# Kernel tuning notes

Hardware: AMD Instinct MI355X
Metric: run time of the kernel (lower is better)

The kernel has to match this reference:

```python
import jax, jax.numpy as jnp
import numpy as np

N = 200000   # gaussians
M = 10000    # scaffold nodes
K = 16       # skinning knn
T = 40       # time steps
F = 32       # semantic feature dim
MAX_S = 0.1
MIN_S = 0.0
EPS = 1e-8


def _qnorm(q):
    return q / jnp.clip(jnp.linalg.norm(q, axis=-1, keepdims=True), 1e-12)


def q2R(q):
    # quaternion (w, x, y, z) -> rotation matrix, normalizing first (matches q2R in source)
    q = _qnorm(q)
    w, x, y, z = q[..., 0], q[..., 1], q[..., 2], q[..., 3]
    r0 = jnp.stack([1 - 2 * (y * y + z * z), 2 * (x * y - w * z), 2 * (x * z + w * y)], -1)
    r1 = jnp.stack([2 * (x * y + w * z), 1 - 2 * (x * x + z * z), 2 * (y * z - w * x)], -1)
    r2 = jnp.stack([2 * (x * z - w * y), 2 * (y * z + w * x), 1 - 2 * (x * x + y * y)], -1)
    return jnp.stack([r0, r1, r2], -2)


def quat_mul(a, b):
    aw, ax, ay, az = a[..., 0], a[..., 1], a[..., 2], a[..., 3]
    bw, bx, by, bz = b[..., 0], b[..., 1], b[..., 2], b[..., 3]
    return jnp.stack([
        aw * bw - ax * bx - ay * by - az * bz,
        aw * bx + ax * bw + ay * bz - az * by,
        aw * by - ax * bz + ay * bw + az * bx,
        aw * bz + ax * by - ay * bx + az * bw], -1)


def quat_conj(q):
    return q * jnp.array([1.0, -1.0, -1.0, -1.0], q.dtype)


def setup_inputs() -> dict:
    key = jax.random.key(0)
    ks = jax.random.split(key, 13)
    return {
        "gs_xyz": 0.05 * jax.random.normal(ks[0], (N, 3), jnp.float32),
        "gs_rotation": jax.random.normal(ks[1], (N, 4), jnp.float32),
        "gs_scaling": jax.random.normal(ks[2], (N, 3), jnp.float32),
        "gs_opacity": jax.random.normal(ks[3], (N, 1), jnp.float32),
        "feat_dc": jax.random.normal(ks[4], (N, 3), jnp.float32),
        "feat_rest": jax.random.normal(ks[5], (N, 9), jnp.float32),
        "node_xyz": jax.random.normal(ks[6], (T, M, 3), jnp.float32),
        "node_quat": jax.random.normal(ks[7], (T, M, 4), jnp.float32),
        "node_sigma": 0.1 + 0.5 * jax.random.uniform(ks[8], (M, 1), jnp.float32),
        "node_sem": jax.random.normal(ks[9], (M, F), jnp.float32),
        "attach_ind": jax.random.randint(ks[10], (N,), 0, M, jnp.int32),
        "ref_time": jax.random.randint(ks[11], (N,), 0, T, jnp.int32),
        "topo_knn": jax.random.randint(ks[12], (M, K), 0, M, jnp.int32),
        "t": 5,
    }


def reference(gs_xyz, gs_rotation, gs_scaling, gs_opacity, feat_dc, feat_rest,
              node_xyz, node_quat, node_sigma, node_sem,
              attach_ind, ref_time, topo_knn, t):
    # --- per-gaussian activated attributes ---
    s = MIN_S + jax.nn.sigmoid(gs_scaling) * (MAX_S - MIN_S)   # s_act
    o = jax.nn.sigmoid(gs_opacity)                              # o_act
    sph = jnp.concatenate([feat_dc, feat_rest], axis=-1)        # [N, 12], full sph order

    # --- leaf-local -> world at ref time (get_xyz / get_R_mtx) ---
    ref_p_attach = node_xyz[ref_time, attach_ind]               # [N,3] async knn gather
    ref_q_attach = node_quat[ref_time, attach_ind]              # [N,4]
    R_ref_attach = q2R(ref_q_attach)                            # [N,3,3]
    x_world = jnp.einsum('nij,nj->ni', R_ref_attach, gs_xyz) + ref_p_attach
    R_world = jnp.einsum('nij,njk->nik', R_ref_attach, q2R(gs_rotation))

    # --- scf.warp: KNN skinning from per-point ref time to target time t ---
    sk_ind = topo_knn[attach_ind]                               # [N,K] neighbor node ids
    p_ref = node_xyz[ref_time[:, None], sk_ind]                 # [N,K,3]
    q_ref = node_quat[ref_time[:, None], sk_ind]                # [N,K,4]
    p_live = node_xyz[t][sk_ind]                                # [N,K,3]
    q_live = node_quat[t][sk_ind]                               # [N,K,4]
    sigma = node_sigma[sk_ind, 0]                               # [N,K]

    diff = x_world[:, None, :] - p_ref                          # [N,K,3]
    dsq = jnp.sum(diff * diff, axis=-1)                         # [N,K]
    w = jnp.exp(-dsq / (2.0 * sigma * sigma + EPS))             # RBF skinning weights
    w = w / (jnp.sum(w, axis=-1, keepdims=True) + EPS)          # [N,K]

    # per-node relative transform ref -> live
    q_rel = quat_mul(_qnorm(q_live), quat_conj(_qnorm(q_ref)))  # [N,K,4]
    R_rel = q2R(q_rel)                                          # [N,K,3,3]
    mu_k = jnp.einsum('nkij,nkj->nki', R_rel, diff) + p_live    # [N,K,3]
    mu_live = jnp.einsum('nk,nki->ni', w, mu_k)                 # [N,3]

    q_blend = jnp.einsum('nk,nkd->nd', w, q_rel)                # blended quaternion
    fr_live = jnp.einsum('nij,njk->nik', q2R(q_blend), R_world) # [N,3,3]

    sem_live = jnp.einsum('nk,nkf->nf', w, node_sem[sk_ind])    # [N,F]

    return mu_live, fr_live, s, o, sph, sem_live
```

## Files before the change

kernel.cpp:

```cpp
#include <hip/hip_runtime.h>

#define KNN 16
#define FSEM 32
#define LPG 4
#define NXCD 8

__device__ __forceinline__ float sigmoidf_(float x) { return 1.0f / (1.0f + __expf(-x)); }

__device__ __forceinline__ void quat_to_R(float qw, float qx, float qy, float qz, float* R) {
    float d = qw * qw + qx * qx + qy * qy + qz * qz;
    float inv = rsqrtf(fmaxf(d, 1e-24f));
    float w = qw * inv, x = qx * inv, y = qy * inv, z = qz * inv;
    R[0] = 1.f - 2.f * (y * y + z * z); R[1] = 2.f * (x * y - w * z); R[2] = 2.f * (x * z + w * y);
    R[3] = 2.f * (x * y + w * z); R[4] = 1.f - 2.f * (x * x + z * z); R[5] = 2.f * (y * z - w * x);
    R[6] = 2.f * (x * z - w * y); R[7] = 2.f * (y * z + w * x); R[8] = 1.f - 2.f * (x * x + y * y);
}

__global__ void __launch_bounds__(256)
k_pack(const float* __restrict__ node_xyz, const float* __restrict__ node_quat,
       const float* __restrict__ node_sigma,
       float* __restrict__ packed, int* __restrict__ cnt, int TM, int M, int B)
{
    int p = blockIdx.x * blockDim.x + threadIdx.x;
    if (p < B && cnt) cnt[p] = 0;
    if (p >= TM) return;
    const int node = p - (p / M) * M;
    const float* x = node_xyz + 3 * (size_t)p;
    float4 a = make_float4(x[0], x[1], x[2], node_sigma[node]);
    float4 q = reinterpret_cast<const float4*>(node_quat)[p];
    float4* dst = reinterpret_cast<float4*>(packed + 8 * (size_t)p);
    dst[0] = a;
    dst[1] = q;
}

__global__ void __launch_bounds__(256)
k_hist(const int* __restrict__ attach, const int* __restrict__ rtime,
       int* __restrict__ cnt, int* __restrict__ rank, int N, int M)
{
    int n = blockIdx.x * blockDim.x + threadIdx.x;
    if (n >= N) return;
    const int key = rtime[n] * M + attach[n];
    rank[n] = atomicAdd(&cnt[key], 1);
}

__global__ void __launch_bounds__(256)
k_scan1(int* __restrict__ cnt, int* __restrict__ blk, int B)
{
    __shared__ int sh[256];
    const int i = blockIdx.x * 256 + threadIdx.x;
    int v = (i < B) ? cnt[i] : 0;
    sh[threadIdx.x] = v;
    __syncthreads();
    int acc = v;
#pragma unroll
    for (int off = 1; off < 256; off <<= 1) {
        int u = (threadIdx.x >= off) ? sh[threadIdx.x - off] : 0;
        __syncthreads();
        acc += u;
        sh[threadIdx.x] = acc;
        __syncthreads();
    }
    if (i < B) cnt[i] = acc - v;
    if (threadIdx.x == 255) blk[blockIdx.x] = acc;
}

__global__ void __launch_bounds__(256)
k_scan2(int* __restrict__ blk, int nblk)
{
    __shared__ int sh[256];
    __shared__ int carry_s;
    if (threadIdx.x == 0) carry_s = 0;
    __syncthreads();
    for (int base = 0; base < nblk; base += 256) {
        const int i = base + threadIdx.x;
        int v = (i < nblk) ? blk[i] : 0;
        sh[threadIdx.x] = v;
        __syncthreads();
        int acc = v;
#pragma unroll
        for (int off = 1; off < 256; off <<= 1) {
            int u = (threadIdx.x >= off) ? sh[threadIdx.x - off] : 0;
            __syncthreads();
            acc += u;
            sh[threadIdx.x] = acc;
            __syncthreads();
        }
        const int carry = carry_s;
        if (i < nblk) blk[i] = acc - v + carry;
        __syncthreads();
        if (threadIdx.x == 255) carry_s = carry + acc;
        __syncthreads();
    }
}

__global__ void __launch_bounds__(256)
k_scatter(const int* __restrict__ attach, const int* __restrict__ rtime,
          const float* __restrict__ gs_xyz,
          const int* __restrict__ rank, const int* __restrict__ cnt,
          const int* __restrict__ blk, float4* __restrict__ meta, int N, int M)
{
    int n = blockIdx.x * blockDim.x + threadIdx.x;
    if (n >= N) return;
    const int a = attach[n], rt = rtime[n];
    const int key = rt * M + a;
    const int pos = cnt[key] + blk[key >> 8] + rank[n];
    meta[2 * (size_t)pos]     = make_float4(__int_as_float(n), __int_as_float(a),
                                            __int_as_float(rt), 0.f);
    meta[2 * (size_t)pos + 1] = make_float4(gs_xyz[3 * (size_t)n + 0],
                                            gs_xyz[3 * (size_t)n + 1],
                                            gs_xyz[3 * (size_t)n + 2], 0.f);
}

template<bool FR>
__global__ void __launch_bounds__(256)
k_elem(const float* __restrict__ gs_scal,
       const float* __restrict__ gs_opa,
       const float* __restrict__ feat_dc,
       const float* __restrict__ feat_rest,
       const float* __restrict__ gs_rot,
       const float* __restrict__ node_quat,
       const int*   __restrict__ attach_ind,
       const int*   __restrict__ ref_time,
       const float* __restrict__ qb_ws,
       float* __restrict__ out, int N, int M)
{
    const int n = blockIdx.x * blockDim.x + threadIdx.x;
    if (n >= N) return;
    const size_t Ns = (size_t)N, ns = (size_t)n;

    float* os = out + 12 * Ns + 3 * ns;
    os[0] = 0.1f * sigmoidf_(gs_scal[3 * ns + 0]);
    os[1] = 0.1f * sigmoidf_(gs_scal[3 * ns + 1]);
    os[2] = 0.1f * sigmoidf_(gs_scal[3 * ns + 2]);

    out[15 * Ns + ns] = sigmoidf_(gs_opa[ns]);

    float* osph = out + 16 * Ns + 12 * ns;
    float4 v0 = make_float4(feat_dc[3 * ns + 0], feat_dc[3 * ns + 1], feat_dc[3 * ns + 2],
                            feat_rest[9 * ns + 0]);
    float4 v1 = make_float4(feat_rest[9 * ns + 1], feat_rest[9 * ns + 2],
                            feat_rest[9 * ns + 3], feat_rest[9 * ns + 4]);
    float4 v2 = make_float4(feat_rest[9 * ns + 5], feat_rest[9 * ns + 6],
                            feat_rest[9 * ns + 7], feat_rest[9 * ns + 8]);
    reinterpret_cast<float4*>(osph)[0] = v0;
    reinterpret_cast<float4*>(osph)[1] = v1;
    reinterpret_cast<float4*>(osph)[2] = v2;

    if constexpr (FR) {
        const int a  = attach_ind[n];
        const int rt = ref_time[n];
        const float4 qa = reinterpret_cast<const float4*>(node_quat)[(size_t)rt * (size_t)M + (size_t)a];
        float Rref[9];
        quat_to_R(qa.x, qa.y, qa.z, qa.w, Rref);

        const float4 qg = reinterpret_cast<const float4*>(gs_rot)[ns];
        float Rg[9];
        quat_to_R(qg.x, qg.y, qg.z, qg.w, Rg);

        float Rw[9];
#pragma unroll
        for (int i = 0; i < 3; i++)
#pragma unroll
            for (int j = 0; j < 3; j++)
                Rw[3 * i + j] = Rref[3 * i] * Rg[j] + Rref[3 * i + 1] * Rg[3 + j] + Rref[3 * i + 2] * Rg[6 + j];

        const float4 qb = reinterpret_cast<const float4*>(qb_ws)[ns];
        float Rb[9];
        quat_to_R(qb.x, qb.y, qb.z, qb.w, Rb);

        float* ofr = out + 3 * Ns + 9 * ns;
#pragma unroll
        for (int i = 0; i < 3; i++)
#pragma unroll
            for (int j = 0; j < 3; j++)
                ofr[3 * i + j] = Rb[3 * i] * Rw[j] + Rb[3 * i + 1] * Rw[3 + j] + Rb[3 * i + 2] * Rw[6 + j];
    }
}

template<bool PACKED, bool FRSPLIT, bool SORTED>
__global__ void __launch_bounds__(256)
dynscf_kernel(const float* __restrict__ gs_xyz,
              const float* __restrict__ gs_rot,
              const float* __restrict__ node_xyz,
              const float* __restrict__ node_quat,
              const float* __restrict__ packed,
              const float* __restrict__ node_sigma,
              const float* __restrict__ node_sem,
              const int* __restrict__ attach_ind,
              const int* __restrict__ ref_time,
              const int* __restrict__ topo_knn,
              const int* __restrict__ t_ptr,
              const float4* __restrict__ meta,
              float* __restrict__ out,
              float* __restrict__ qb_out,
              int N, int M)
{
    int bid = blockIdx.x;
    if (SORTED) {
        const int nwg = gridDim.x;
        const int q = nwg / NXCD, r = nwg % NXCD;
        const int xcd = bid % NXCD, idx = bid / NXCD;
        bid = (xcd < r ? xcd * (q + 1) : r * (q + 1) + (xcd - r) * q) + idx;
    }
    const int tid = bid * blockDim.x + threadIdx.x;
    const int g   = tid >> 2;
    const int sub = tid & (LPG - 1);
    if (g >= N) return;

    const int t = t_ptr[0];

    int n, a, rt;
    float gx, gy, gz;
    if (SORTED) {
        const float4 m0 = meta[2 * (size_t)g];
        const float4 m1 = meta[2 * (size_t)g + 1];
        n  = __float_as_int(m0.x);
        a  = __float_as_int(m0.y);
        rt = __float_as_int(m0.z);
        gx = m1.x; gy = m1.y; gz = m1.z;
    } else {
        n  = g;
        a  = attach_ind[n];
        rt = ref_time[n];
        gx = gs_xyz[3 * (size_t)n + 0];
        gy = gs_xyz[3 * (size_t)n + 1];
        gz = gs_xyz[3 * (size_t)n + 2];
    }

    const size_t base_rt = (size_t)rt * (size_t)M;
    const size_t base_t  = (size_t)t  * (size_t)M;

    const int4 kv = reinterpret_cast<const int4*>(topo_knn)[(size_t)a * (KNN / 4) + sub];
    const int js[4] = { kv.x, kv.y, kv.z, kv.w };

    float apx, apy, apz, aqw, aqx, aqy, aqz;
    if (PACKED) {
        const float4* pk = reinterpret_cast<const float4*>(packed + (base_rt + (size_t)a) * 8);
        float4 xz = pk[0], qv = pk[1];
        apx = xz.x; apy = xz.y; apz = xz.z;
        aqw = qv.x; aqx = qv.y; aqy = qv.z; aqz = qv.w;
    } else {
        const float4 qv = *reinterpret_cast<const float4*>(node_quat + (base_rt + (size_t)a) * 4);
        const float* pa = node_xyz + (base_rt + (size_t)a) * 3;
        apx = pa[0]; apy = pa[1]; apz = pa[2];
        aqw = qv.x; aqx = qv.y; aqy = qv.z; aqz = qv.w;
    }
    float Rref[9];
    quat_to_R(aqw, aqx, aqy, aqz, Rref);

    const float xw0 = Rref[0] * gx + Rref[1] * gy + Rref[2] * gz + apx;
    const float xw1 = Rref[3] * gx + Rref[4] * gy + Rref[5] * gz + apy;
    const float xw2 = Rref[6] * gx + Rref[7] * gy + Rref[8] * gz + apz;

    float wsum = 0.f, mu0 = 0.f, mu1 = 0.f, mu2 = 0.f;
    float qb0 = 0.f, qb1 = 0.f, qb2 = 0.f, qb3 = 0.f;
    float wk[4];

#pragma unroll
    for (int k = 0; k < KNN / LPG; k++) {
        const int j = js[k];

        float prx, pry, prz, rw, rx, ry, rz;
        float plx, ply, plz, lw, lx, ly, lz;
        float sg;
        if (PACKED) {
            const float4* pkr = reinterpret_cast<const float4*>(packed + (base_rt + (size_t)j) * 8);
            float4 xr = pkr[0], qr = pkr[1];
            prx = xr.x; pry = xr.y; prz = xr.z; sg = xr.w;
            rw = qr.x; rx = qr.y; ry = qr.z; rz = qr.w;
            const float4* pkl = reinterpret_cast<const float4*>(packed + (base_t + (size_t)j) * 8);
            float4 xl = pkl[0], ql = pkl[1];
            plx = xl.x; ply = xl.y; plz = xl.z;
            lw = ql.x; lx = ql.y; ly = ql.z; lz = ql.w;
        } else {
            const float* pr = node_xyz + (base_rt + (size_t)j) * 3;
            prx = pr[0]; pry = pr[1]; prz = pr[2];
            const float4 qr = *reinterpret_cast<const float4*>(node_quat + (base_rt + (size_t)j) * 4);
            rw = qr.x; rx = qr.y; ry = qr.z; rz = qr.w;
            const float* pl = node_xyz + (base_t + (size_t)j) * 3;
            plx = pl[0]; ply = pl[1]; plz = pl[2];
            const float4 ql = *reinterpret_cast<const float4*>(node_quat + (base_t + (size_t)j) * 4);
            lw = ql.x; lx = ql.y; ly = ql.z; lz = ql.w;
            sg = node_sigma[j];
        }

        const float dx = xw0 - prx;
        const float dy = xw1 - pry;
        const float dz = xw2 - prz;
        const float dsq = dx * dx + dy * dy + dz * dz;

        const float w = __expf(-dsq / (2.f * sg * sg + 1e-8f));
        wk[k] = w;

        {
            float inv = rsqrtf(fmaxf(rw * rw + rx * rx + ry * ry + rz * rz, 1e-24f));
            rw *= inv; rx *= inv; ry *= inv; rz *= inv;
        }
        {
            float inv = rsqrtf(fmaxf(lw * lw + lx * lx + ly * ly + lz * lz, 1e-24f));
            lw *= inv; lx *= inv; ly *= inv; lz *= inv;
        }
        const float qw =  lw * rw + lx * rx + ly * ry + lz * rz;
        const float qx = -lw * rx + lx * rw - ly * rz + lz * ry;
        const float qy = -lw * ry + lx * rz + ly * rw - lz * rx;
        const float qz = -lw * rz - lx * ry + ly * rx + lz * rw;

        float Rr[9];
        quat_to_R(qw, qx, qy, qz, Rr);

        const float m0 = Rr[0] * dx + Rr[1] * dy + Rr[2] * dz + plx;
        const float m1 = Rr[3] * dx + Rr[4] * dy + Rr[5] * dz + ply;
        const float m2 = Rr[6] * dx + Rr[7] * dy + Rr[8] * dz + plz;

        wsum += w;
        mu0 += w * m0; mu1 += w * m1; mu2 += w * m2;
        qb0 += w * qw; qb1 += w * qx; qb2 += w * qy; qb3 += w * qz;
    }

#pragma unroll
    for (int m = 1; m < LPG; m <<= 1) {
        wsum += __shfl_xor(wsum, m);
        mu0  += __shfl_xor(mu0, m);  mu1 += __shfl_xor(mu1, m);  mu2 += __shfl_xor(mu2, m);
        qb0  += __shfl_xor(qb0, m);  qb1 += __shfl_xor(qb1, m);
        qb2  += __shfl_xor(qb2, m);  qb3 += __shfl_xor(qb3, m);
    }

    const float invw = 1.f / (wsum + 1e-8f);
    const size_t Ns = (size_t)N, ns = (size_t)n;

    float sm0 = 0.f, sm1 = 0.f, sm2 = 0.f, sm3 = 0.f;
    float sm4 = 0.f, sm5 = 0.f, sm6 = 0.f, sm7 = 0.f;
    const float4* sem4 = reinterpret_cast<const float4*>(node_sem);
#pragma unroll
    for (int kk = 0; kk < KNN; kk++) {
        const int src = kk >> 2;
        const int idx = kk & 3;
        const int   jk = __shfl(js[idx], src, LPG);
        const float wkk = __shfl(wk[idx], src, LPG);
        const float4 v0 = sem4[(size_t)jk * (FSEM / 4) + sub * 2 + 0];
        const float4 v1 = sem4[(size_t)jk * (FSEM / 4) + sub * 2 + 1];
        sm0 += wkk * v0.x; sm1 += wkk * v0.y; sm2 += wkk * v0.z; sm3 += wkk * v0.w;
        sm4 += wkk * v1.x; sm5 += wkk * v1.y; sm6 += wkk * v1.z; sm7 += wkk * v1.w;
    }

    if (sub == 0) {
        out[3 * ns + 0] = mu0 * invw;
        out[3 * ns + 1] = mu1 * invw;
        out[3 * ns + 2] = mu2 * invw;
    } else if (sub == 1) {
        if (FRSPLIT) {
            reinterpret_cast<float4*>(qb_out)[ns] =
                make_float4(qb0 * invw, qb1 * invw, qb2 * invw, qb3 * invw);
        }
    }

    if constexpr (!FRSPLIT) {
        if (sub == 1) {
            const float4 qg = *reinterpret_cast<const float4*>(gs_rot + 4 * ns);
            float Rg[9];
            quat_to_R(qg.x, qg.y, qg.z, qg.w, Rg);
            float Rw[9];
#pragma unroll
            for (int i = 0; i < 3; i++)
#pragma unroll
                for (int j = 0; j < 3; j++)
                    Rw[3 * i + j] = Rref[3 * i] * Rg[j] + Rref[3 * i + 1] * Rg[3 + j] + Rref[3 * i + 2] * Rg[6 + j];
            float Rb[9];
            quat_to_R(qb0 * invw, qb1 * invw, qb2 * invw, qb3 * invw, Rb);
            float* ofr = out + 3 * Ns + 9 * ns;
#pragma unroll
            for (int i = 0; i < 3; i++)
#pragma unroll
                for (int j = 0; j < 3; j++)
                    ofr[3 * i + j] = Rb[3 * i] * Rw[j] + Rb[3 * i + 1] * Rw[3 + j] + Rb[3 * i + 2] * Rw[6 + j];
        }
    }

    float4* osem = reinterpret_cast<float4*>(out + 28 * Ns + FSEM * ns);
    osem[sub * 2 + 0] = make_float4(sm0 * invw, sm1 * invw, sm2 * invw, sm3 * invw);
    osem[sub * 2 + 1] = make_float4(sm4 * invw, sm5 * invw, sm6 * invw, sm7 * invw);
}

extern "C" void kernel_launch(void* const* d_in, const int* in_sizes, int n_in,
                              void* d_out, int out_size, void* d_ws, size_t ws_size,
                              hipStream_t stream)
{
    const float* gs_xyz     = (const float*)d_in[0];
    const float* gs_rot     = (const float*)d_in[1];
    const float* gs_scal    = (const float*)d_in[2];
    const float* gs_opa     = (const float*)d_in[3];
    const float* feat_dc    = (const float*)d_in[4];
    const float* feat_rest  = (const float*)d_in[5];
    const float* node_xyz   = (const float*)d_in[6];
    const float* node_quat  = (const float*)d_in[7];
    const float* node_sigma = (const float*)d_in[8];
    const float* node_sem   = (const float*)d_in[9];
    const int* attach_ind   = (const int*)d_in[10];
    const int* ref_time     = (const int*)d_in[11];
    const int* topo_knn     = (const int*)d_in[12];
    const int* t_ptr        = (const int*)d_in[13];

    const int N = in_sizes[0] / 3;
    const int M = in_sizes[8];
    const int TM = in_sizes[6] / 3;
    const int B  = TM;

    float* out = (float*)d_out;

    const int block = 256;
    const int gridN = (N + block - 1) / block;
    const long long threads = (long long)N * LPG;
    const int gridM = (int)((threads + block - 1) / block);
    const int gridP = (TM + block - 1) / block;
    const int nblkS = (B + 255) / 256;

    const size_t f_packed = (size_t)TM * 8;
    const size_t f_qb     = (size_t)N * 4;
    const size_t f_meta   = (size_t)N * 8;
    const size_t i_cnt    = (size_t)B;
    const size_t i_blk    = 4096;
    const size_t need_sort   = (f_packed + f_qb + f_meta + i_cnt + i_blk) * sizeof(float);
    const size_t need_packed = (f_packed + f_qb) * sizeof(float);
    const size_t need_qb     = f_qb * sizeof(float);

    if (ws_size >= need_sort && nblkS <= 4096) {
        float*  packed = (float*)d_ws;
        float*  qb_ws  = packed + f_packed;
        float4* meta   = (float4*)(packed + f_packed + f_qb);
        int*    cnt    = (int*)(packed + f_packed + f_qb + f_meta);
        int*    blk    = cnt + i_cnt;
        int*    rank   = (int*)qb_ws;

        hipLaunchKernelGGL(k_pack, dim3(gridP), dim3(block), 0, stream,
                           node_xyz, node_quat, node_sigma, packed, cnt, TM, M, B);
        hipLaunchKernelGGL(k_hist, dim3(gridN), dim3(block), 0, stream,
                           attach_ind, ref_time, cnt, rank, N, M);
        hipLaunchKernelGGL(k_scan1, dim3(nblkS), dim3(block), 0, stream,
                           cnt, blk, B);
        hipLaunchKernelGGL(k_scan2, dim3(1), dim3(block), 0, stream,
                           blk, nblkS);
        hipLaunchKernelGGL(k_scatter, dim3(gridN), dim3(block), 0, stream,
                           attach_ind, ref_time, gs_xyz, rank, cnt, blk, meta, N, M);
        hipLaunchKernelGGL((dynscf_kernel<true, true, true>), dim3(gridM), dim3(block), 0, stream,
                           gs_xyz, gs_rot, node_xyz, node_quat, packed, node_sigma, node_sem,
                           attach_ind, ref_time, topo_knn, t_ptr, meta, out, qb_ws, N, M);
        hipLaunchKernelGGL((k_elem<true>), dim3(gridN), dim3(block), 0, stream,
                           gs_scal, gs_opa, feat_dc, feat_rest, gs_rot, node_quat,
                           attach_ind, ref_time, qb_ws, out, N, M);
    } else if (ws_size >= need_packed) {
        float* packed = (float*)d_ws;
        float* qb_ws  = packed + f_packed;
        hipLaunchKernelGGL(k_pack, dim3(gridP), dim3(block), 0, stream,
                           node_xyz, node_quat, node_sigma, packed, (int*)nullptr, TM, M, 0);
        hipLaunchKernelGGL((dynscf_kernel<true, true, false>), dim3(gridM), dim3(block), 0, stream,
                           gs_xyz, gs_rot, node_xyz, node_quat, packed, node_sigma, node_sem,
                           attach_ind, ref_time, topo_knn, t_ptr, (const float4*)nullptr,
                           out, qb_ws, N, M);
        hipLaunchKernelGGL((k_elem<true>), dim3(gridN), dim3(block), 0, stream,
                           gs_scal, gs_opa, feat_dc, feat_rest, gs_rot, node_quat,
                           attach_ind, ref_time, qb_ws, out, N, M);
    } else if (ws_size >= need_qb) {
        float* qb_ws = (float*)d_ws;
        hipLaunchKernelGGL((dynscf_kernel<false, true, false>), dim3(gridM), dim3(block), 0, stream,
                           gs_xyz, gs_rot, node_xyz, node_quat, (const float*)nullptr,
                           node_sigma, node_sem,
                           attach_ind, ref_time, topo_knn, t_ptr, (const float4*)nullptr,
                           out, qb_ws, N, M);
        hipLaunchKernelGGL((k_elem<true>), dim3(gridN), dim3(block), 0, stream,
                           gs_scal, gs_opa, feat_dc, feat_rest, gs_rot, node_quat,
                           attach_ind, ref_time, qb_ws, out, N, M);
    } else {
        hipLaunchKernelGGL((dynscf_kernel<false, false, false>), dim3(gridM), dim3(block), 0, stream,
                           gs_xyz, gs_rot, node_xyz, node_quat, (const float*)nullptr,
                           node_sigma, node_sem,
                           attach_ind, ref_time, topo_knn, t_ptr, (const float4*)nullptr,
                           out, (float*)nullptr, N, M);
        hipLaunchKernelGGL((k_elem<false>), dim3(gridN), dim3(block), 0, stream,
                           gs_scal, gs_opa, feat_dc, feat_rest, gs_rot, node_quat,
                           attach_ind, ref_time, (const float*)nullptr, out, N, M);
    }
}
```

Before: 215.5 us.

## Coarsen sort keys to time-by-node-bucket and fuse pack with histogram

The counting sort that groups gaussians now keys on (ref_time, attach>>shift) with 256 buckets per time step instead of the full (time, node) key. This shrinks the histogram enough for a single-block scan, so the two-level scan and the blk array go away. The pack and histogram kernels are merged, counters are cleared with a memset, and the main kernel gains a launch-bounds occupancy hint. Coarser buckets give weaker gather locality inside the main kernel, and the extra atomic contention on fewer counters could offset the savings from fewer launches.

```diff
diff --git a/kernel.cpp b/kernel.cpp
--- a/kernel.cpp
+++ b/kernel.cpp
@@ -4,6 +4,7 @@
 #define FSEM 32
 #define LPG 4
 #define NXCD 8
+#define NSUB 256
 
 __device__ __forceinline__ float sigmoidf_(float x) { return 1.0f / (1.0f + __expf(-x)); }
 
@@ -17,63 +18,38 @@
 }
 
 __global__ void __launch_bounds__(256)
-k_pack(const float* __restrict__ node_xyz, const float* __restrict__ node_quat,
-       const float* __restrict__ node_sigma,
-       float* __restrict__ packed, int* __restrict__ cnt, int TM, int M, int B)
+k_pack_hist(const float* __restrict__ node_xyz, const float* __restrict__ node_quat,
+            const float* __restrict__ node_sigma,
+            const int* __restrict__ attach, const int* __restrict__ rtime,
+            float* __restrict__ packed, int* __restrict__ cnt, int* __restrict__ rank,
+            int TM, int M, int N, int shift)
 {
     int p = blockIdx.x * blockDim.x + threadIdx.x;
-    if (p < B && cnt) cnt[p] = 0;
-    if (p >= TM) return;
-    const int node = p - (p / M) * M;
-    const float* x = node_xyz + 3 * (size_t)p;
-    float4 a = make_float4(x[0], x[1], x[2], node_sigma[node]);
-    float4 q = reinterpret_cast<const float4*>(node_quat)[p];
-    float4* dst = reinterpret_cast<float4*>(packed + 8 * (size_t)p);
-    dst[0] = a;
-    dst[1] = q;
+    if (p < TM) {
+        const int node = p - (p / M) * M;
+        const float* x = node_xyz + 3 * (size_t)p;
+        float4 a = make_float4(x[0], x[1], x[2], node_sigma[node]);
+        float4 q = reinterpret_cast<const float4*>(node_quat)[p];
+        float4* dst = reinterpret_cast<float4*>(packed + 8 * (size_t)p);
+        dst[0] = a;
+        dst[1] = q;
+    }
+    if (p < N && cnt) {
+        const int key = rtime[p] * NSUB + (attach[p] >> shift);
+        rank[p] = atomicAdd(&cnt[key], 1);
+    }
 }
 
 __global__ void __launch_bounds__(256)
-k_hist(const int* __restrict__ attach, const int* __restrict__ rtime,
-       int* __restrict__ cnt, int* __restrict__ rank, int N, int M)
-{
-    int n = blockIdx.x * blockDim.x + threadIdx.x;
-    if (n >= N) return;
-    const int key = rtime[n] * M + attach[n];
-    rank[n] = atomicAdd(&cnt[key], 1);
-}
-
-__global__ void __launch_bounds__(256)
-k_scan1(int* __restrict__ cnt, int* __restrict__ blk, int B)
-{
-    __shared__ int sh[256];
-    const int i = blockIdx.x * 256 + threadIdx.x;
-    int v = (i < B) ? cnt[i] : 0;
-    sh[threadIdx.x] = v;
-    __syncthreads();
-    int acc = v;
-#pragma unroll
-    for (int off = 1; off < 256; off <<= 1) {
-        int u = (threadIdx.x >= off) ? sh[threadIdx.x - off] : 0;
-        __syncthreads();
-        acc += u;
-        sh[threadIdx.x] = acc;
-        __syncthreads();
-    }
-    if (i < B) cnt[i] = acc - v;
-    if (threadIdx.x == 255) blk[blockIdx.x] = acc;
-}
-
-__global__ void __launch_bounds__(256)
-k_scan2(int* __restrict__ blk, int nblk)
+k_scan(int* __restrict__ cnt, int B)
 {
     __shared__ int sh[256];
     __shared__ int carry_s;
     if (threadIdx.x == 0) carry_s = 0;
     __syncthreads();
-    for (int base = 0; base < nblk; base += 256) {
+    for (int base = 0; base < B; base += 256) {
         const int i = base + threadIdx.x;
-        int v = (i < nblk) ? blk[i] : 0;
+        int v = (i < B) ? cnt[i] : 0;
         sh[threadIdx.x] = v;
         __syncthreads();
         int acc = v;
@@ -86,7 +62,7 @@
             __syncthreads();
         }
         const int carry = carry_s;
-        if (i < nblk) blk[i] = acc - v + carry;
+        if (i < B) cnt[i] = acc - v + carry;
         __syncthreads();
         if (threadIdx.x == 255) carry_s = carry + acc;
         __syncthreads();
@@ -97,13 +73,13 @@
 k_scatter(const int* __restrict__ attach, const int* __restrict__ rtime,
           const float* __restrict__ gs_xyz,
           const int* __restrict__ rank, const int* __restrict__ cnt,
-          const int* __restrict__ blk, float4* __restrict__ meta, int N, int M)
+          float4* __restrict__ meta, int N, int shift)
 {
     int n = blockIdx.x * blockDim.x + threadIdx.x;
     if (n >= N) return;
     const int a = attach[n], rt = rtime[n];
-    const int key = rt * M + a;
-    const int pos = cnt[key] + blk[key >> 8] + rank[n];
+    const int key = rt * NSUB + (a >> shift);
+    const int pos = cnt[key] + rank[n];
     meta[2 * (size_t)pos]     = make_float4(__int_as_float(n), __int_as_float(a),
                                             __int_as_float(rt), 0.f);
     meta[2 * (size_t)pos + 1] = make_float4(gs_xyz[3 * (size_t)n + 0],
@@ -178,7 +154,7 @@
 }
 
 template<bool PACKED, bool FRSPLIT, bool SORTED>
-__global__ void __launch_bounds__(256)
+__global__ void __launch_bounds__(256, 8)
 dynscf_kernel(const float* __restrict__ gs_xyz,
               const float* __restrict__ gs_rot,
               const float* __restrict__ node_xyz,
@@ -403,7 +379,11 @@
     const int N = in_sizes[0] / 3;
     const int M = in_sizes[8];
     const int TM = in_sizes[6] / 3;
-    const int B  = TM;
+    const int T  = TM / M;
+    const int B  = T * NSUB;
+
+    int shift = 0;
+    while (((M - 1) >> shift) >= NSUB) shift++;
 
     float* out = (float*)d_out;
 
@@ -411,36 +391,30 @@
     const int gridN = (N + block - 1) / block;
     const long long threads = (long long)N * LPG;
     const int gridM = (int)((threads + block - 1) / block);
-    const int gridP = (TM + block - 1) / block;
-    const int nblkS = (B + 255) / 256;
+    const int gridPH = (((TM > N ? TM : N)) + block - 1) / block;
 
     const size_t f_packed = (size_t)TM * 8;
     const size_t f_qb     = (size_t)N * 4;
     const size_t f_meta   = (size_t)N * 8;
     const size_t i_cnt    = (size_t)B;
-    const size_t i_blk    = 4096;
-    const size_t need_sort   = (f_packed + f_qb + f_meta + i_cnt + i_blk) * sizeof(float);
+    const size_t need_sort   = (f_packed + f_qb + f_meta + i_cnt) * sizeof(float);
     const size_t need_packed = (f_packed + f_qb) * sizeof(float);
     const size_t need_qb     = f_qb * sizeof(float);
 
-    if (ws_size >= need_sort && nblkS <= 4096) {
+    if (ws_size >= need_sort) {
         float*  packed = (float*)d_ws;
         float*  qb_ws  = packed + f_packed;
         float4* meta   = (float4*)(packed + f_packed + f_qb);
         int*    cnt    = (int*)(packed + f_packed + f_qb + f_meta);
-        int*    blk    = cnt + i_cnt;
         int*    rank   = (int*)qb_ws;
 
-        hipLaunchKernelGGL(k_pack, dim3(gridP), dim3(block), 0, stream,
-                           node_xyz, node_quat, node_sigma, packed, cnt, TM, M, B);
-        hipLaunchKernelGGL(k_hist, dim3(gridN), dim3(block), 0, stream,
-                           attach_ind, ref_time, cnt, rank, N, M);
-        hipLaunchKernelGGL(k_scan1, dim3(nblkS), dim3(block), 0, stream,
-                           cnt, blk, B);
-        hipLaunchKernelGGL(k_scan2, dim3(1), dim3(block), 0, stream,
-                           blk, nblkS);
+        hipMemsetAsync(cnt, 0, (size_t)B * sizeof(int), stream);
+        hipLaunchKernelGGL(k_pack_hist, dim3(gridPH), dim3(block), 0, stream,
+                           node_xyz, node_quat, node_sigma, attach_ind, ref_time,
+                           packed, cnt, rank, TM, M, N, shift);
+        hipLaunchKernelGGL(k_scan, dim3(1), dim3(block), 0, stream, cnt, B);
         hipLaunchKernelGGL(k_scatter, dim3(gridN), dim3(block), 0, stream,
-                           attach_ind, ref_time, gs_xyz, rank, cnt, blk, meta, N, M);
+                           attach_ind, ref_time, gs_xyz, rank, cnt, meta, N, shift);
         hipLaunchKernelGGL((dynscf_kernel<true, true, true>), dim3(gridM), dim3(block), 0, stream,
                            gs_xyz, gs_rot, node_xyz, node_quat, packed, node_sigma, node_sem,
                            attach_ind, ref_time, topo_knn, t_ptr, meta, out, qb_ws, N, M);
@@ -450,8 +424,9 @@
     } else if (ws_size >= need_packed) {
         float* packed = (float*)d_ws;
         float* qb_ws  = packed + f_packed;
-        hipLaunchKernelGGL(k_pack, dim3(gridP), dim3(block), 0, stream,
-                           node_xyz, node_quat, node_sigma, packed, (int*)nullptr, TM, M, 0);
+        hipLaunchKernelGGL(k_pack_hist, dim3(gridPH), dim3(block), 0, stream,
+                           node_xyz, node_quat, node_sigma, attach_ind, ref_time,
+                           packed, (int*)nullptr, (int*)nullptr, TM, M, 0, shift);
         hipLaunchKernelGGL((dynscf_kernel<true, true, false>), dim3(gridM), dim3(block), 0, stream,
                            gs_xyz, gs_rot, node_xyz, node_quat, packed, node_sigma, node_sem,
                            attach_ind, ref_time, topo_knn, t_ptr, (const float4*)nullptr,
```

New measurement: 477.3 us. +121.4%, slower.
